# Kernel tuning notes

Measured on AMD Instinct MI355X. Metric: run time of the kernel, lower is better.

## Reference

```python
import jax, jax.numpy as jnp
import numpy as np

NEG = 0.01  # LeakyReLU default slope
EPS = 1e-5  # InstanceNorm eps

def conv(x, w, b=None, pad=0, groups=1):
    y = jax.lax.conv_general_dilated(x, w, (1, 1), [(pad, pad), (pad, pad)],
                                     dimension_numbers=('NCHW', 'OIHW', 'NCHW'),
                                     feature_group_count=groups)
    if b is not None:
        y = y + b[None, :, None, None]
    return y

def inorm(x):
    m = jnp.mean(x, axis=(2, 3), keepdims=True)
    v = jnp.var(x, axis=(2, 3), keepdims=True)
    return (x - m) / jnp.sqrt(v + EPS)

def lrelu(x):
    return jax.nn.leaky_relu(x, NEG)

def maxpool2(x):
    return jax.lax.reduce_window(x, -jnp.inf, jax.lax.max, (1, 1, 2, 2), (1, 1, 2, 2), 'VALID')

def setup_inputs() -> dict:
    key = jax.random.key(0)
    ks = jax.random.split(key, 17)
    C = 64
    def w(k, shape, fan_in):
        return (jax.random.normal(k, shape, jnp.float32) * (1.0 / np.sqrt(fan_in)))
    return {
        'x': jax.random.normal(ks[0], (4, 3, 256, 256), jnp.float32),
        'w_proj': w(ks[1], (C, 3, 3, 3), 27), 'b_proj': jnp.zeros((C,), jnp.float32),
        'w_a1': w(ks[2], (C // 4, C, 1, 1), C), 'w_a2': w(ks[3], (C, C // 4, 1, 1), C // 4),
        'w_ref': w(ks[4], (C, 1, 3, 3), 9), 'b_ref': jnp.zeros((C,), jnp.float32),
        'w_fuse': w(ks[5], (C, C, 1, 1), C), 'b_fuse': jnp.zeros((C,), jnp.float32),
        'w_con': w(ks[6], (2 * C * 4, 1, 3, 3), 9),
        'w_u1': w(ks[7], (C, 2 * C * 4, 1, 1), 2 * C * 4), 'b_u1': jnp.zeros((C,), jnp.float32),
        'w_u2': w(ks[8], (C, C, 3, 3), 9 * C), 'b_u2': jnp.zeros((C,), jnp.float32),
        'w_sc': w(ks[9], (C, 2 * C, 1, 1), 2 * C), 'b_sc': jnp.zeros((C,), jnp.float32),
    }

def reference(x, w_proj, b_proj, w_a1, w_a2, w_ref, b_ref, w_fuse, b_fuse,
              w_con, w_u1, b_u1, w_u2, b_u2, w_sc, b_sc):
    xp = conv(x, w_proj, b_proj, pad=1)
    B, C, H, W = xp.shape
    # --- high branch: pywt wavedec2+waverec2 is perfect reconstruction (identity);
    #     torch code detaches -> stop_gradient on the reconstruction path
    xw = jax.lax.stop_gradient(xp)
    a = jnp.mean(xw, axis=(2, 3), keepdims=True)          # AdaptiveAvgPool2d(1)
    a = lrelu(conv(a, w_a1))
    a = jax.nn.sigmoid(conv(a, w_a2))
    xw = xw * a
    xw = conv(xw, w_ref, b_ref, pad=1, groups=C)          # depthwise refine
    xw = lrelu(inorm(xw))
    # --- low branch: FFT low-pass box filter
    f = jnp.fft.fftshift(jnp.fft.fft2(xp), axes=(-2, -1))
    hl = int(H * 0.3 // 2); wl = int(W * 0.3 // 2)
    hc, wc = H // 2, W // 2
    mask = jnp.zeros((H, W), bool).at[hc - hl:hc + hl, wc - wl:wc + wl].set(True)
    low = jnp.fft.ifft2(jnp.fft.ifftshift(f * mask, axes=(-2, -1))).real
    low = lrelu(inorm(conv(low, w_fuse, b_fuse)))
    # --- hypergraph construct / unwrap
    xc = jnp.concatenate([xw, low], axis=1)               # [B, 2C, H, W]
    h = conv(xc, w_con, pad=1, groups=2 * C)              # [B, 2C*k, H, W]
    u = lrelu(inorm(conv(h, w_u1, b_u1)))
    u = lrelu(inorm(conv(u, w_u2, b_u2, pad=1)))
    feat = u + conv(xc, w_sc, b_sc)
    pooled = maxpool2(feat)
    return feat, pooled
```

## Files before the change

kernel.cpp:

```cpp
#include <hip/hip_runtime.h>
#include <hip/hip_bf16.h>

#define WIDTH 256
#define HW 65536
#define IMG 16777216
#define NIMG 256
#define NSPLIT 16

typedef __attribute__((ext_vector_type(8))) short bf8v;
typedef __attribute__((ext_vector_type(4))) float f4v;

__device__ __forceinline__ float lrelu_f(float v){ return v > 0.f ? v : 0.01f*v; }
__device__ __forceinline__ unsigned short bf16u(float v){
    __hip_bfloat16 h = __float2bfloat16(v);
    return *(unsigned short*)&h;
}

__global__ __launch_bounds__(256) void k_statsf(const float* __restrict__ ps, float* __restrict__ st)
{
    const int img = threadIdx.x;
    const float* p = ps + blockIdx.x * (256 * NSPLIT * 2) + img * (NSPLIT * 2);
    float* o = st + blockIdx.x * 512;
    float S = 0.f, S2 = 0.f;
#pragma unroll
    for (int q = 0; q < NSPLIT; q++) { S += p[q * 2]; S2 += p[q * 2 + 1]; }
    const float m = S / 65536.f;
    const float var = S2 / 65536.f - m * m;
    o[img * 2]     = m;
    o[img * 2 + 1] = rsqrtf(var + 1e-5f);
}

__global__ __launch_bounds__(256) void k_attention(const float* __restrict__ ps0,
    const float* __restrict__ wa1, const float* __restrict__ wa2, float* __restrict__ a2o)
{
    __shared__ float means[256];
    __shared__ float a1s[64];
    const int tid = threadIdx.x;
    {
        const float* p = ps0 + tid * (NSPLIT * 2);
        float S = 0.f;
#pragma unroll
        for (int q = 0; q < NSPLIT; q++) S += p[q * 2];
        means[tid] = S * (1.f / 65536.f);
    }
    __syncthreads();
    if (tid < 64) {
        const int b = tid >> 4, o = tid & 15;
        float s = 0.f;
        for (int c = 0; c < 64; c++) s += wa1[o * 64 + c] * means[b * 64 + c];
        a1s[b * 16 + o] = lrelu_f(s);
    }
    __syncthreads();
    {
        const int b = tid >> 6, c = tid & 63;
        float s = 0.f;
#pragma unroll
        for (int o = 0; o < 16; o++) s += wa2[c * 16 + o] * a1s[b * 16 + o];
        a2o[tid] = 1.f / (1.f + expf(-s));
    }
}

__global__ __launch_bounds__(256, 3) void k_proj(const float* __restrict__ x,
    const float* __restrict__ wt, const float* __restrict__ bias,
    float* __restrict__ out, float* __restrict__ ps0)
{
    __shared__ float wl[3][9][32];
    const int tid = threadIdx.x;
    const int og = tid >> 5, xg = tid & 31;
    const int half = blockIdx.x & 1;
    const int y = (blockIdx.x >> 1) & 255;
    const int b = blockIdx.x >> 9;
    const int o_base = half * 32;
    const int o0l = og * 4;
    const int x0 = xg * 8;
    const int split = y & (NSPLIT - 1);

    for (int idx = tid; idx < 3 * 9 * 32; idx += 256) {
        const int o = idx & 31;
        const int rest = idx >> 5;
        const int pos = rest % 9, cc = rest / 9;
        wl[cc][pos][o] = wt[((o_base + o) * 3 + cc) * 9 + pos];
    }
    __syncthreads();

    float acc[4][8];
#pragma unroll
    for (int i = 0; i < 4; i++)
#pragma unroll
        for (int j = 0; j < 8; j++) acc[i][j] = 0.f;

#pragma unroll 2
    for (int cc = 0; cc < 3; cc++) {
        const float* src = x + ((size_t)b * 3 + cc) * HW;
#pragma unroll
        for (int dy = 0; dy < 3; dy++) {
            const int yy = y + dy - 1;
            float vv[10];
            if (yy >= 0 && yy < 256) {
                const float* r = src + (size_t)yy * WIDTH;
                vv[0] = (x0 > 0) ? r[x0 - 1] : 0.f;
                const float4 m0 = *(const float4*)(r + x0);
                const float4 m1 = *(const float4*)(r + x0 + 4);
                vv[1] = m0.x; vv[2] = m0.y; vv[3] = m0.z; vv[4] = m0.w;
                vv[5] = m1.x; vv[6] = m1.y; vv[7] = m1.z; vv[8] = m1.w;
                vv[9] = (x0 < 248) ? r[x0 + 8] : 0.f;
            } else {
#pragma unroll
                for (int q = 0; q < 10; q++) vv[q] = 0.f;
            }
#pragma unroll
            for (int dx = 0; dx < 3; dx++) {
                const float4 w4 = *(const float4*)&wl[cc][dy * 3 + dx][o0l];
                const float wv[4] = { w4.x, w4.y, w4.z, w4.w };
#pragma unroll
                for (int oi = 0; oi < 4; oi++)
#pragma unroll
                    for (int px = 0; px < 8; px++)
                        acc[oi][px] += wv[oi] * vv[px + dx];
            }
        }
    }
#pragma unroll
    for (int oi = 0; oi < 4; oi++) {
        const int o = o_base + o0l + oi;
        const float bv = bias[o];
        const size_t off = ((size_t)(b * 64 + o)) * HW + (size_t)y * WIDTH + x0;
        float4 r0, r1;
        r0.x = acc[oi][0] + bv; r0.y = acc[oi][1] + bv; r0.z = acc[oi][2] + bv; r0.w = acc[oi][3] + bv;
        r1.x = acc[oi][4] + bv; r1.y = acc[oi][5] + bv; r1.z = acc[oi][6] + bv; r1.w = acc[oi][7] + bv;
        *(float4*)(out + off) = r0;
        *(float4*)(out + off + 4) = r1;
        float s  = r0.x + r0.y + r0.z + r0.w + r1.x + r1.y + r1.z + r1.w;
        float s2 = r0.x*r0.x + r0.y*r0.y + r0.z*r0.z + r0.w*r0.w
                 + r1.x*r1.x + r1.y*r1.y + r1.z*r1.z + r1.w*r1.w;
#pragma unroll
        for (int offt = 16; offt > 0; offt >>= 1) {
            s  += __shfl_down(s, offt, 32);
            s2 += __shfl_down(s2, offt, 32);
        }
        if (xg == 0) {
            float* pp = &ps0[((b * 64 + o) * NSPLIT + split) * 2];
            atomicAdd(pp, s);
            atomicAdd(pp + 1, s2);
        }
    }
}

__global__ __launch_bounds__(256) void k_dw(const float* __restrict__ xp, const float* __restrict__ a2,
    const float* __restrict__ wref, const float* __restrict__ bref, float* __restrict__ out,
    float* __restrict__ ps1)
{
    const int tid = threadIdx.x;
    const int img = blockIdx.x >> 6;
    const int y = ((blockIdx.x & 63) << 2) + (tid >> 6);
    const int x0 = (tid & 63) * 4;
    const int c = img & 63;
    const int split = blockIdx.x & (NSPLIT - 1);
    const float* src = xp + (size_t)img * HW;
    float wv[9];
#pragma unroll
    for (int k = 0; k < 9; k++) wv[k] = wref[c * 9 + k];
    const float scale = a2[img], bb = bref[c];

    float a[4] = {0.f, 0.f, 0.f, 0.f};
#pragma unroll
    for (int dy = 0; dy < 3; dy++) {
        const int yy = y + dy - 1;
        if (yy < 0 || yy > 255) continue;
        const float* r = src + (size_t)yy * WIDTH;
        float vv[6];
        vv[0] = (x0 > 0) ? r[x0 - 1] : 0.f;
        const float4 m = *(const float4*)(r + x0);
        vv[1] = m.x; vv[2] = m.y; vv[3] = m.z; vv[4] = m.w;
        vv[5] = (x0 < 252) ? r[x0 + 4] : 0.f;
#pragma unroll
        for (int dx = 0; dx < 3; dx++)
#pragma unroll
            for (int px = 0; px < 4; px++)
                a[px] += wv[dy * 3 + dx] * vv[px + dx];
    }
    float4 o;
    o.x = bb + scale * a[0]; o.y = bb + scale * a[1];
    o.z = bb + scale * a[2]; o.w = bb + scale * a[3];
    *(float4*)(out + (size_t)img * HW + (size_t)y * WIDTH + x0) = o;

    float s  = o.x + o.y + o.z + o.w;
    float s2 = o.x*o.x + o.y*o.y + o.z*o.z + o.w*o.w;
#pragma unroll
    for (int offt = 32; offt > 0; offt >>= 1) {
        s  += __shfl_down(s, offt, 64);
        s2 += __shfl_down(s2, offt, 64);
    }
    __shared__ float ls[4][2];
    const int wid = tid >> 6, lane = tid & 63;
    if (lane == 0) { ls[wid][0] = s; ls[wid][1] = s2; }
    __syncthreads();
    if (tid == 0) {
        const float S  = ls[0][0] + ls[1][0] + ls[2][0] + ls[3][0];
        const float S2 = ls[0][1] + ls[1][1] + ls[2][1] + ls[3][1];
        float* pp = &ps1[(img * NSPLIT + split) * 2];
        atomicAdd(pp, S);
        atomicAdd(pp + 1, S2);
    }
}

__global__ void k_tables(float* __restrict__ kr2, float* __restrict__ ki2)
{
    const int t = blockIdx.x * 256 + threadIdx.x;
    if (t < 512) {
        const int tm = t & 255;
        const double PI = 3.14159265358979323846;
        const double th = 2.0 * PI * (double)tm / 256.0;
        double sr = 1.0;
        for (int k = 1; k <= 37; k++) sr += 2.0 * cos((double)k * th);
        sr += cos(38.0 * th);
        kr2[t] = (float)(sr / 256.0);
        ki2[t] = (float)(-sin(38.0 * th) / 256.0);
    }
}

__global__ __launch_bounds__(256) void k_kmat(const float* __restrict__ kr2, const float* __restrict__ ki2,
    unsigned short* __restrict__ KBr, unsigned short* __restrict__ KBi)
{
    const int n = blockIdx.x, k = threadIdx.x;
    const int d = (n - k) & 255;
    KBr[n * 256 + k] = bf16u(kr2[d]);
    KBi[n * 256 + k] = bf16u(ki2[d]);
}

__global__ __launch_bounds__(256, 2) void k_mdft1(const float* __restrict__ xp,
    const unsigned short* __restrict__ KBr, const unsigned short* __restrict__ KBi,
    unsigned short* __restrict__ TR, unsigned short* __restrict__ TI)
{
    const int tid = threadIdx.x, lane = tid & 63, wave = tid >> 6;
    const int img = blockIdx.x >> 2;
    const int mb = (blockIdx.x >> 1) & 1, nb = blockIdx.x & 1;
    const int M0 = mb * 128 + (wave >> 1) * 64;
    const int N0 = nb * 128 + (wave & 1) * 64;
    const int lrow = lane & 15, lk = lane >> 4;
    const float* Xb = xp + (size_t)img * HW;

    f4v aR[4][4], aI[4][4];
#pragma unroll
    for (int m = 0; m < 4; m++)
#pragma unroll
        for (int n = 0; n < 4; n++) { aR[m][n] = (f4v){0,0,0,0}; aI[m][n] = (f4v){0,0,0,0}; }

#pragma unroll 1
    for (int k0 = 0; k0 < 256; k0 += 32) {
        bf8v af[4];
#pragma unroll
        for (int m = 0; m < 4; m++) {
            const float* rp = Xb + (size_t)(M0 + m * 16 + lrow) * 256 + k0 + lk * 8;
            const float4 a0 = *(const float4*)rp;
            const float4 a1 = *(const float4*)(rp + 4);
            bf8v t;
            t[0] = (short)bf16u(a0.x); t[1] = (short)bf16u(a0.y);
            t[2] = (short)bf16u(a0.z); t[3] = (short)bf16u(a0.w);
            t[4] = (short)bf16u(a1.x); t[5] = (short)bf16u(a1.y);
            t[6] = (short)bf16u(a1.z); t[7] = (short)bf16u(a1.w);
            af[m] = t;
        }
#pragma unroll
        for (int n = 0; n < 4; n++) {
            const int xcol = N0 + n * 16 + lrow;
            const bf8v br = *(const bf8v*)(KBr + xcol * 256 + k0 + lk * 8);
            const bf8v bi = *(const bf8v*)(KBi + xcol * 256 + k0 + lk * 8);
#pragma unroll
            for (int m = 0; m < 4; m++) {
                aR[m][n] = __builtin_amdgcn_mfma_f32_16x16x32_bf16(af[m], br, aR[m][n], 0, 0, 0);
                aI[m][n] = __builtin_amdgcn_mfma_f32_16x16x32_bf16(af[m], bi, aI[m][n], 0, 0, 0);
            }
        }
    }
#pragma unroll
    for (int n = 0; n < 4; n++) {
        const size_t xoff = (size_t)img * HW + (size_t)(N0 + n * 16 + lrow) * 256;
#pragma unroll
        for (int m = 0; m < 4; m++) {
            const size_t off = xoff + M0 + m * 16 + lk * 4;
            const f4v r = aR[m][n], ii = aI[m][n];
            ushort4 ur, ui;
            ur.x = bf16u(r[0]); ur.y = bf16u(r[1]); ur.z = bf16u(r[2]); ur.w = bf16u(r[3]);
            ui.x = bf16u(ii[0]); ui.y = bf16u(ii[1]); ui.z = bf16u(ii[2]); ui.w = bf16u(ii[3]);
            *(ushort4*)(TR + off) = ur;
            *(ushort4*)(TI + off) = ui;
        }
    }
}

__global__ __launch_bounds__(256, 2) void k_mdft2(const unsigned short* __restrict__ TR,
    const unsigned short* __restrict__ TI, const unsigned short* __restrict__ KBr,
    const unsigned short* __restrict__ KBi, float* __restrict__ low)
{
    const int tid = threadIdx.x, lane = tid & 63, wave = tid >> 6;
    const int img = blockIdx.x >> 2;
    const int mb = (blockIdx.x >> 1) & 1, nb = blockIdx.x & 1;
    const int M0 = mb * 128 + (wave >> 1) * 64;
    const int N0 = nb * 128 + (wave & 1) * 64;
    const int lrow = lane & 15, lk = lane >> 4;
    const unsigned short* TRb = TR + (size_t)img * HW;
    const unsigned short* TIb = TI + (size_t)img * HW;

    f4v aR[4][4], aI[4][4];
#pragma unroll
    for (int m = 0; m < 4; m++)
#pragma unroll
        for (int n = 0; n < 4; n++) { aR[m][n] = (f4v){0,0,0,0}; aI[m][n] = (f4v){0,0,0,0}; }

#pragma unroll 1
    for (int k0 = 0; k0 < 256; k0 += 32) {
        bf8v afR[4], afI[4];
#pragma unroll
        for (int m = 0; m < 4; m++) {
            const int ro = (M0 + m * 16 + lrow) * 256 + k0 + lk * 8;
            afR[m] = *(const bf8v*)(TRb + ro);
            afI[m] = *(const bf8v*)(TIb + ro);
        }
#pragma unroll
        for (int n = 0; n < 4; n++) {
            const int ycol = N0 + n * 16 + lrow;
            const bf8v br = *(const bf8v*)(KBr + ycol * 256 + k0 + lk * 8);
            const bf8v bi = *(const bf8v*)(KBi + ycol * 256 + k0 + lk * 8);
#pragma unroll
            for (int m = 0; m < 4; m++) {
                aR[m][n] = __builtin_amdgcn_mfma_f32_16x16x32_bf16(afR[m], br, aR[m][n], 0, 0, 0);
                aI[m][n] = __builtin_amdgcn_mfma_f32_16x16x32_bf16(afI[m], bi, aI[m][n], 0, 0, 0);
            }
        }
    }
#pragma unroll
    for (int n = 0; n < 4; n++) {
        const size_t yoff = (size_t)img * HW + (size_t)(N0 + n * 16 + lrow) * 256;
#pragma unroll
        for (int m = 0; m < 4; m++) {
            const f4v r = aR[m][n], ii = aI[m][n];
            const float4 v = make_float4(r[0] - ii[0], r[1] - ii[1], r[2] - ii[2], r[3] - ii[3]);
            *(float4*)(low + yoff + M0 + m * 16 + lk * 4) = v;
        }
    }
}

__global__ __launch_bounds__(256) void k_weff_bf(const float* __restrict__ w_u1,
    const float* __restrict__ w_con, unsigned short* __restrict__ wbf)
{
    const int f = blockIdx.x * 256 + threadIdx.x;
    if (f >= 73728) return;
    const int ch = f & 31, oc = (f >> 5) & 63, cp = f >> 11;
    const int pos = cp % 9, cb = cp / 9;
    const int g = cb * 32 + ch;
    float s = 0.f;
#pragma unroll
    for (int j = 0; j < 4; j++) s += w_u1[oc * 512 + g * 4 + j] * w_con[(g * 4 + j) * 9 + pos];
    wbf[f] = bf16u(s);
}

template<int CIN>
__global__ __launch_bounds__(256) void k_wcvt(const float* __restrict__ w, unsigned short* __restrict__ wbf)
{
    const int f = blockIdx.x * 256 + threadIdx.x;
    if (f >= 64 * CIN * 9) return;
    const int ch = f & 31, oc = (f >> 5) & 63, cp = f >> 11;
    const int pos = cp % 9, cb = cp / 9;
    const int c = cb * 32 + ch;
    wbf[f] = bf16u(w[oc * CIN * 9 + c * 9 + pos]);
}

template<int CIN>
__global__ __launch_bounds__(256) void k_wcvt1(const float* __restrict__ w, unsigned short* __restrict__ wbf)
{
    const int f = blockIdx.x * 256 + threadIdx.x;
    if (f >= 64 * CIN) return;
    const int ch = f & 31, oc = (f >> 5) & 63, cb = f >> 11;
    wbf[f] = bf16u(w[oc * CIN + cb * 32 + ch]);
}

template<int CIN>
__global__ __launch_bounds__(256, 2) void k_mconv(
    const float* __restrict__ in0, const float* __restrict__ in1,
    const unsigned short* __restrict__ wbf, const float* __restrict__ bias,
    float* __restrict__ out,
    const float* __restrict__ stA, const float* __restrict__ stB,
    float* __restrict__ psOut)
{
    __shared__ unsigned short Xl[4 * 260 * 32];
    __shared__ float sh_ms[64];
    __shared__ float red[4][64][2];
    const int tid = threadIdx.x;
    const int lane = tid & 63;
    const int wave = tid >> 6;
    const int b = blockIdx.x >> 7;
    const int y0 = (blockIdx.x & 127) * 2;
    const int row_sel = wave >> 1;
    const int px_base = (wave & 1) * 128;
    const int split = blockIdx.x & (NSPLIT - 1);

    for (int i = tid; i < 4 * 260 * 32 / 2; i += 256) ((unsigned int*)Xl)[i] = 0u;

    f4v acc[8][4];
#pragma unroll
    for (int i = 0; i < 8; i++)
#pragma unroll
        for (int n = 0; n < 4; n++) acc[i][n] = (f4v){0.f, 0.f, 0.f, 0.f};

    const int pxl   = px_base + (lane & 15);
    const int gsl   = lane >> 4;
    const int wlane = (lane & 15) * 32 + gsl * 8;

    constexpr int NC = CIN / 32;
#pragma unroll 1
    for (int cb = 0; cb < NC; cb++) {
        const int c0 = cb * 32;
        const bool second = (CIN == 128 && c0 >= 64);
        const float* src = (second ? in1 : in0) + ((size_t)b * 64 + (c0 & 63)) * HW;
        const float* st = second ? stB : stA;
        __syncthreads();
        if (tid < 32) {
            const int img = b * 64 + (c0 & 63) + tid;
            sh_ms[tid * 2]     = st[img * 2];
            sh_ms[tid * 2 + 1] = st[img * 2 + 1];
        }
        __syncthreads();
        {
            const int px = tid;
            const int px_idx = px + 1;
            const int sw = (px_idx >> 1) & 3;
#pragma unroll 1
            for (int r = 0; r < 4; r++) {
                const int yy = y0 - 1 + r;
                if (yy < 0 || yy > 255) continue;
                const float* rp = src + (size_t)yy * WIDTH + px;
#pragma unroll 4
                for (int d = 0; d < 16; d++) {
                    float va = rp[(size_t)(2 * d) * HW];
                    float vb = rp[(size_t)(2 * d + 1) * HW];
                    va = lrelu_f((va - sh_ms[4 * d])     * sh_ms[4 * d + 1]);
                    vb = lrelu_f((vb - sh_ms[4 * d + 2]) * sh_ms[4 * d + 3]);
                    const unsigned int dw = (unsigned int)bf16u(va)
                                          | ((unsigned int)bf16u(vb) << 16);
                    const int byte = r * 16640 + px_idx * 64
                                   + (((d >> 2) ^ sw) << 4) + ((d & 3) << 2);
                    *(unsigned int*)((char*)Xl + byte) = dw;
                }
            }
        }
        __syncthreads();
#pragma unroll 1
        for (int pos = 0; pos < 9; pos++) {
            const int dy = pos / 3, dx = pos - dy * 3;
            const unsigned short* wp = wbf + (cb * 9 + pos) * 2048 + wlane;
            const bf8v wf0 = *(const bf8v*)(wp);
            const bf8v wf1 = *(const bf8v*)(wp + 512);
            const bf8v wf2 = *(const bf8v*)(wp + 1024);
            const bf8v wf3 = *(const bf8v*)(wp + 1536);
            const int pxe = pxl + dx;
            const int row = row_sel + dy;
            const char* abase = (const char*)Xl + row * 16640 + pxe * 64
                              + ((gsl ^ ((pxe >> 1) & 3)) << 4);
#pragma unroll
            for (int i = 0; i < 8; i++) {
                const bf8v af = *(const bf8v*)(abase + i * 1024);
                acc[i][0] = __builtin_amdgcn_mfma_f32_16x16x32_bf16(af, wf0, acc[i][0], 0, 0, 0);
                acc[i][1] = __builtin_amdgcn_mfma_f32_16x16x32_bf16(af, wf1, acc[i][1], 0, 0, 0);
                acc[i][2] = __builtin_amdgcn_mfma_f32_16x16x32_bf16(af, wf2, acc[i][2], 0, 0, 0);
                acc[i][3] = __builtin_amdgcn_mfma_f32_16x16x32_bf16(af, wf3, acc[i][3], 0, 0, 0);
            }
        }
    }
    const int yrow = y0 + row_sel;
    const int lrow = lane & 15, lk = lane >> 4;
#pragma unroll
    for (int n = 0; n < 4; n++) {
        const float bv = bias[n * 16 + lrow];
        float* po = out + ((size_t)(b * 64) + n * 16 + lrow) * HW
                  + (size_t)yrow * WIDTH + px_base + lk * 4;
        float s = 0.f, s2 = 0.f;
#pragma unroll
        for (int i = 0; i < 8; i++) {
            const f4v a = acc[i][n];
            float4 v;
            v.x = a[0] + bv; v.y = a[1] + bv; v.z = a[2] + bv; v.w = a[3] + bv;
            s  += v.x + v.y + v.z + v.w;
            s2 += v.x*v.x + v.y*v.y + v.z*v.z + v.w*v.w;
            *(float4*)(po + i * 16) = v;
        }
        s  += __shfl_down(s, 32);  s  += __shfl_down(s, 16);
        s2 += __shfl_down(s2, 32); s2 += __shfl_down(s2, 16);
        if (lk == 0) { red[wave][n * 16 + lrow][0] = s; red[wave][n * 16 + lrow][1] = s2; }
    }
    __syncthreads();
    if (tid < 64) {
        const float S  = red[0][tid][0] + red[1][tid][0] + red[2][tid][0] + red[3][tid][0];
        const float S2 = red[0][tid][1] + red[1][tid][1] + red[2][tid][1] + red[3][tid][1];
        float* pp = &psOut[((b * 64 + tid) * NSPLIT + split) * 2];
        atomicAdd(pp, S);
        atomicAdd(pp + 1, S2);
    }
}

template<int CIN, bool ADD, bool NORMIN, bool STATS>
__global__ __launch_bounds__(256, 2) void k_pconv(
    const float* __restrict__ in0, const float* __restrict__ in1,
    const unsigned short* __restrict__ wbf, const float* __restrict__ bias,
    const float* __restrict__ addsrc, float* __restrict__ out,
    const float* __restrict__ stA, const float* __restrict__ stB,
    const float* __restrict__ stAdd, float* __restrict__ psOut)
{
    __shared__ unsigned short Xl[256 * 32];
    __shared__ float sh_ms[64];
    __shared__ float red[4][64][2];
    const int tid = threadIdx.x, lane = tid & 63, wave = tid >> 6;
    const int y = blockIdx.x & 255, b = blockIdx.x >> 8;
    const int split = blockIdx.x & (NSPLIT - 1);
    const int lrow = lane & 15, gsl = lane >> 4;
    const int wpx = wave * 64;
    const int wlane = lrow * 32 + gsl * 8;

    f4v acc[4][4];
#pragma unroll
    for (int m = 0; m < 4; m++)
#pragma unroll
        for (int n = 0; n < 4; n++) acc[m][n] = (f4v){0.f, 0.f, 0.f, 0.f};

    constexpr int NC = CIN / 32;
#pragma unroll 1
    for (int cb = 0; cb < NC; cb++) {
        const int c0 = cb * 32;
        const bool second = (CIN == 128 && c0 >= 64);
        const float* src = (second ? in1 : in0) + ((size_t)b * 64 + (c0 & 63)) * HW
                         + (size_t)y * WIDTH;
        __syncthreads();
        if (NORMIN && tid < 32) {
            const float* st = second ? stB : stA;
            const int img = b * 64 + (c0 & 63) + tid;
            sh_ms[tid * 2]     = st[img * 2];
            sh_ms[tid * 2 + 1] = st[img * 2 + 1];
        }
        __syncthreads();
        {
            const int px = tid;
            const int sw = (px >> 1) & 3;
#pragma unroll 4
            for (int d = 0; d < 16; d++) {
                float va = src[(size_t)(2 * d) * HW + px];
                float vb = src[(size_t)(2 * d + 1) * HW + px];
                if constexpr (NORMIN) {
                    va = lrelu_f((va - sh_ms[4 * d])     * sh_ms[4 * d + 1]);
                    vb = lrelu_f((vb - sh_ms[4 * d + 2]) * sh_ms[4 * d + 3]);
                }
                const unsigned int dw = (unsigned int)bf16u(va)
                                      | ((unsigned int)bf16u(vb) << 16);
                const int byte = px * 64 + (((d >> 2) ^ sw) << 4) + ((d & 3) << 2);
                *(unsigned int*)((char*)Xl + byte) = dw;
            }
        }
        __syncthreads();
        {
            const unsigned short* wp = wbf + cb * 2048 + wlane;
            const bf8v wf0 = *(const bf8v*)(wp);
            const bf8v wf1 = *(const bf8v*)(wp + 512);
            const bf8v wf2 = *(const bf8v*)(wp + 1024);
            const bf8v wf3 = *(const bf8v*)(wp + 1536);
#pragma unroll
            for (int m = 0; m < 4; m++) {
                const int px = wpx + m * 16 + lrow;
                const char* abase = (const char*)Xl + px * 64
                                  + ((gsl ^ ((px >> 1) & 3)) << 4);
                const bf8v af = *(const bf8v*)abase;
                acc[m][0] = __builtin_amdgcn_mfma_f32_16x16x32_bf16(af, wf0, acc[m][0], 0, 0, 0);
                acc[m][1] = __builtin_amdgcn_mfma_f32_16x16x32_bf16(af, wf1, acc[m][1], 0, 0, 0);
                acc[m][2] = __builtin_amdgcn_mfma_f32_16x16x32_bf16(af, wf2, acc[m][2], 0, 0, 0);
                acc[m][3] = __builtin_amdgcn_mfma_f32_16x16x32_bf16(af, wf3, acc[m][3], 0, 0, 0);
            }
        }
    }
    const int lk = gsl;
#pragma unroll
    for (int n = 0; n < 4; n++) {
        const int oc = n * 16 + lrow;
        const float bv = bias[oc];
        float mm = 0.f, ss = 0.f;
        if constexpr (ADD) { mm = stAdd[(b * 64 + oc) * 2]; ss = stAdd[(b * 64 + oc) * 2 + 1]; }
        const size_t orow = ((size_t)(b * 64 + oc)) * HW + (size_t)y * WIDTH;
        float s = 0.f, s2 = 0.f;
#pragma unroll
        for (int m = 0; m < 4; m++) {
            const int px = wpx + m * 16 + lk * 4;
            const f4v a = acc[m][n];
            float r[4] = { a[0] + bv, a[1] + bv, a[2] + bv, a[3] + bv };
            if constexpr (ADD) {
                const float4 av = *(const float4*)(addsrc + orow + px);
                r[0] += lrelu_f((av.x - mm) * ss);
                r[1] += lrelu_f((av.y - mm) * ss);
                r[2] += lrelu_f((av.z - mm) * ss);
                r[3] += lrelu_f((av.w - mm) * ss);
            }
            *(float4*)(out + orow + px) = make_float4(r[0], r[1], r[2], r[3]);
            if constexpr (STATS) {
                s  += r[0] + r[1] + r[2] + r[3];
                s2 += r[0]*r[0] + r[1]*r[1] + r[2]*r[2] + r[3]*r[3];
            }
        }
        if constexpr (STATS) {
            s  += __shfl_down(s, 32);  s  += __shfl_down(s, 16);
            s2 += __shfl_down(s2, 32); s2 += __shfl_down(s2, 16);
            if (lk == 0) { red[wave][oc][0] = s; red[wave][oc][1] = s2; }
        }
    }
    if constexpr (STATS) {
        __syncthreads();
        if (tid < 64) {
            const float S  = red[0][tid][0] + red[1][tid][0] + red[2][tid][0] + red[3][tid][0];
            const float S2 = red[0][tid][1] + red[1][tid][1] + red[2][tid][1] + red[3][tid][1];
            float* pp = &psOut[((b * 64 + tid) * NSPLIT + split) * 2];
            atomicAdd(pp, S);
            atomicAdd(pp + 1, S2);
        }
    }
}

__global__ __launch_bounds__(256) void k_maxpool(const float* __restrict__ feat, float* __restrict__ out)
{
    const int idx = blockIdx.x * 256 + threadIdx.x;
    const int xo = idx & 127;
    const int yo = (idx >> 7) & 127;
    const int img = idx >> 14;
    const float* p = feat + (size_t)img * HW + (size_t)(yo * 2) * WIDTH + xo * 2;
    out[idx] = fmaxf(fmaxf(p[0], p[1]), fmaxf(p[WIDTH], p[WIDTH + 1]));
}

extern "C" void kernel_launch(void* const* d_in, const int* in_sizes, int n_in,
                              void* d_out, int out_size, void* d_ws, size_t ws_size,
                              hipStream_t stream)
{
    const float* x      = (const float*)d_in[0];
    const float* w_proj = (const float*)d_in[1];
    const float* b_proj = (const float*)d_in[2];
    const float* w_a1   = (const float*)d_in[3];
    const float* w_a2   = (const float*)d_in[4];
    const float* w_ref  = (const float*)d_in[5];
    const float* b_ref  = (const float*)d_in[6];
    const float* w_fuse = (const float*)d_in[7];
    const float* b_fuse = (const float*)d_in[8];
    const float* w_con  = (const float*)d_in[9];
    const float* w_u1   = (const float*)d_in[10];
    const float* b_u1   = (const float*)d_in[11];
    const float* w_u2   = (const float*)d_in[12];
    const float* b_u2   = (const float*)d_in[13];
    const float* w_sc   = (const float*)d_in[14];
    const float* b_sc   = (const float*)d_in[15];

    float* wsf  = (float*)d_ws;
    float* buf0 = wsf;
    float* buf1 = wsf + (size_t)IMG;
    float* buf2 = wsf + (size_t)2 * IMG;
    float* aux  = wsf + (size_t)3 * IMG;
    float* a2b  = aux;
    float* kr2  = aux + 256;
    float* ki2  = aux + 768;
    unsigned short* wbfA = (unsigned short*)(aux + 1280);
    unsigned short* wbfB = wbfA + 73728;
    unsigned short* KBr  = wbfB + 36864;
    unsigned short* KBi  = KBr + 65536;
    unsigned short* wbfF = KBi + 65536;
    unsigned short* wbfS = wbfF + 4096;
    float* ps   = aux + 1280 + 120832 + 6144;
    float* st   = ps + 5 * 256 * NSPLIT * 2;

    float* fout = (float*)d_out;
    float* pout = fout + (size_t)IMG;
    unsigned short* T1R = (unsigned short*)buf2;
    unsigned short* T1I = T1R + (size_t)IMG;

    const int PSSLOT = 256 * NSPLIT * 2;

    hipMemsetAsync(ps, 0, 5 * PSSLOT * sizeof(float), stream);
    k_tables<<<2, 256, 0, stream>>>(kr2, ki2);
    k_kmat<<<256, 256, 0, stream>>>(kr2, ki2, KBr, KBi);
    k_weff_bf<<<288, 256, 0, stream>>>(w_u1, w_con, wbfA);
    k_wcvt<64><<<144, 256, 0, stream>>>(w_u2, wbfB);
    k_wcvt1<64><<<16, 256, 0, stream>>>(w_fuse, wbfF);
    k_wcvt1<128><<<32, 256, 0, stream>>>(w_sc, wbfS);
    k_proj<<<2048, 256, 0, stream>>>(x, w_proj, b_proj, buf0, ps);
    k_attention<<<1, 256, 0, stream>>>(ps, w_a1, w_a2, a2b);
    k_dw<<<16384, 256, 0, stream>>>(buf0, a2b, w_ref, b_ref, buf1, ps + PSSLOT);
    k_mdft1<<<1024, 256, 0, stream>>>(buf0, KBr, KBi, T1R, T1I);
    k_mdft2<<<1024, 256, 0, stream>>>(T1R, T1I, KBr, KBi, fout);
    k_pconv<64, false, false, true><<<1024, 256, 0, stream>>>(
        fout, nullptr, wbfF, b_fuse, nullptr, buf0,
        nullptr, nullptr, nullptr, ps + 2 * PSSLOT);
    k_statsf<<<2, 256, 0, stream>>>(ps + PSSLOT, st + 512);
    k_mconv<128><<<512, 256, 0, stream>>>(buf1, buf0, wbfA, b_u1, fout,
        st + 512, st + 1024, ps + 3 * PSSLOT);
    k_statsf<<<1, 256, 0, stream>>>(ps + 3 * PSSLOT, st + 1536);
    k_mconv<64><<<512, 256, 0, stream>>>(fout, nullptr, wbfB, b_u2, buf2,
        st + 1536, st + 1536, ps + 4 * PSSLOT);
    k_statsf<<<1, 256, 0, stream>>>(ps + 4 * PSSLOT, st + 2048);
    k_pconv<128, true, true, false><<<1024, 256, 0, stream>>>(
        buf1, buf0, wbfS, b_sc, buf2, fout,
        st + 512, st + 1024, st + 2048, nullptr);
    k_maxpool<<<16384, 256, 0, stream>>>(fout, pout);
}
```

Baseline: 493.3 us.

## Halve mconv tile width, raise occupancy, preload norm stats once

k_mconv now processes half a row (128 px) per block with a 130-pixel halo tile, halving accumulators and LDS so launch bounds can allow 4 blocks per CU, and the grid doubles to 1024 blocks. Both mconv and pconv load all per-channel mean/scale stats into shared memory once up front, which removes two barriers per channel block and leaves one barrier at the end of each iteration. Narrower tiles re-read halo columns, and only two of four thread groups' row slots are used per staging pass, which may lower load efficiency.

```diff
diff --git a/kernel.cpp b/kernel.cpp
--- a/kernel.cpp
+++ b/kernel.cpp
@@ -376,36 +376,45 @@
 }
 
 template<int CIN>
-__global__ __launch_bounds__(256, 2) void k_mconv(
+__global__ __launch_bounds__(256, 4) void k_mconv(
     const float* __restrict__ in0, const float* __restrict__ in1,
     const unsigned short* __restrict__ wbf, const float* __restrict__ bias,
     float* __restrict__ out,
     const float* __restrict__ stA, const float* __restrict__ stB,
     float* __restrict__ psOut)
 {
-    __shared__ unsigned short Xl[4 * 260 * 32];
-    __shared__ float sh_ms[64];
+    __shared__ unsigned short Xl[4 * 132 * 32];
+    __shared__ float sh_ms[2 * CIN];
     __shared__ float red[4][64][2];
     const int tid = threadIdx.x;
     const int lane = tid & 63;
     const int wave = tid >> 6;
-    const int b = blockIdx.x >> 7;
-    const int y0 = (blockIdx.x & 127) * 2;
+    const int xb = (blockIdx.x & 1) * 128;
+    const int y0 = ((blockIdx.x >> 1) & 127) * 2;
+    const int b = blockIdx.x >> 8;
     const int row_sel = wave >> 1;
-    const int px_base = (wave & 1) * 128;
+    const int px_half = (wave & 1) * 64;
     const int split = blockIdx.x & (NSPLIT - 1);
 
-    for (int i = tid; i < 4 * 260 * 32 / 2; i += 256) ((unsigned int*)Xl)[i] = 0u;
-
-    f4v acc[8][4];
-#pragma unroll
-    for (int i = 0; i < 8; i++)
+    for (int i = tid; i < 4 * 132 * 32 / 2; i += 256) ((unsigned int*)Xl)[i] = 0u;
+    for (int j = tid; j < 2 * CIN; j += 256) {
+        const int cb_ = j >> 6, jj = j & 63;
+        const int c = cb_ * 32 + 2 * (jj >> 2) + ((jj & 3) >> 1);
+        const float* st = (CIN == 128 && cb_ >= 2) ? stB : stA;
+        sh_ms[j] = st[(b * 64 + (c & 63)) * 2 + (jj & 1)];
+    }
+
+    f4v acc[4][4];
+#pragma unroll
+    for (int i = 0; i < 4; i++)
 #pragma unroll
         for (int n = 0; n < 4; n++) acc[i][n] = (f4v){0.f, 0.f, 0.f, 0.f};
 
-    const int pxl   = px_base + (lane & 15);
-    const int gsl   = lane >> 4;
-    const int wlane = (lane & 15) * 32 + gsl * 8;
+    const int lrow = lane & 15;
+    const int gsl  = lane >> 4;
+    const int wlane = lrow * 32 + gsl * 8;
+
+    __syncthreads();
 
     constexpr int NC = CIN / 32;
 #pragma unroll 1
@@ -413,34 +422,30 @@
         const int c0 = cb * 32;
         const bool second = (CIN == 128 && c0 >= 64);
         const float* src = (second ? in1 : in0) + ((size_t)b * 64 + (c0 & 63)) * HW;
-        const float* st = second ? stB : stA;
-        __syncthreads();
-        if (tid < 32) {
-            const int img = b * 64 + (c0 & 63) + tid;
-            sh_ms[tid * 2]     = st[img * 2];
-            sh_ms[tid * 2 + 1] = st[img * 2 + 1];
-        }
-        __syncthreads();
+        const float* ms = sh_ms + cb * 64;
         {
-            const int px = tid;
-            const int px_idx = px + 1;
-            const int sw = (px_idx >> 1) & 3;
+            const int r = tid >> 6;
+            const int yy = y0 - 1 + r;
+            if (yy >= 0 && yy <= 255) {
 #pragma unroll 1
-            for (int r = 0; r < 4; r++) {
-                const int yy = y0 - 1 + r;
-                if (yy < 0 || yy > 255) continue;
-                const float* rp = src + (size_t)yy * WIDTH + px;
+                for (int s = tid & 63; s < 130; s += 64) {
+                    const int x = xb + s - 1;
+                    if (x >= 0 && x <= 255) {
+                        const float* rp = src + (size_t)yy * WIDTH + x;
+                        const int sbase = r * 8448 + s * 64;
+                        const int sw = (s >> 1) & 3;
 #pragma unroll 4
-                for (int d = 0; d < 16; d++) {
-                    float va = rp[(size_t)(2 * d) * HW];
-                    float vb = rp[(size_t)(2 * d + 1) * HW];
-                    va = lrelu_f((va - sh_ms[4 * d])     * sh_ms[4 * d + 1]);
-                    vb = lrelu_f((vb - sh_ms[4 * d + 2]) * sh_ms[4 * d + 3]);
-                    const unsigned int dw = (unsigned int)bf16u(va)
-                                          | ((unsigned int)bf16u(vb) << 16);
-                    const int byte = r * 16640 + px_idx * 64
-                                   + (((d >> 2) ^ sw) << 4) + ((d & 3) << 2);
-                    *(unsigned int*)((char*)Xl + byte) = dw;
+                        for (int d = 0; d < 16; d++) {
+                            float va = rp[(size_t)(2 * d) * HW];
+                            float vb = rp[(size_t)(2 * d + 1) * HW];
+                            va = lrelu_f((va - ms[4 * d])     * ms[4 * d + 1]);
+                            vb = lrelu_f((vb - ms[4 * d + 2]) * ms[4 * d + 3]);
+                            const unsigned int dw = (unsigned int)bf16u(va)
+                                                  | ((unsigned int)bf16u(vb) << 16);
+                            *(unsigned int*)((char*)Xl + sbase
+                                + (((d >> 2) ^ sw) << 4) + ((d & 3) << 2)) = dw;
+                        }
+                    }
                 }
             }
         }
@@ -453,12 +458,12 @@
             const bf8v wf1 = *(const bf8v*)(wp + 512);
             const bf8v wf2 = *(const bf8v*)(wp + 1024);
             const bf8v wf3 = *(const bf8v*)(wp + 1536);
-            const int pxe = pxl + dx;
+            const int pxe = px_half + lrow + dx;
             const int row = row_sel + dy;
-            const char* abase = (const char*)Xl + row * 16640 + pxe * 64
+            const char* abase = (const char*)Xl + row * 8448 + pxe * 64
                               + ((gsl ^ ((pxe >> 1) & 3)) << 4);
 #pragma unroll
-            for (int i = 0; i < 8; i++) {
+            for (int i = 0; i < 4; i++) {
                 const bf8v af = *(const bf8v*)(abase + i * 1024);
                 acc[i][0] = __builtin_amdgcn_mfma_f32_16x16x32_bf16(af, wf0, acc[i][0], 0, 0, 0);
                 acc[i][1] = __builtin_amdgcn_mfma_f32_16x16x32_bf16(af, wf1, acc[i][1], 0, 0, 0);
@@ -466,17 +471,18 @@
                 acc[i][3] = __builtin_amdgcn_mfma_f32_16x16x32_bf16(af, wf3, acc[i][3], 0, 0, 0);
             }
         }
+        __syncthreads();
     }
     const int yrow = y0 + row_sel;
-    const int lrow = lane & 15, lk = lane >> 4;
+    const int lk = gsl;
 #pragma unroll
     for (int n = 0; n < 4; n++) {
         const float bv = bias[n * 16 + lrow];
         float* po = out + ((size_t)(b * 64) + n * 16 + lrow) * HW
-                  + (size_t)yrow * WIDTH + px_base + lk * 4;
+                  + (size_t)yrow * WIDTH + xb + px_half + lk * 4;
         float s = 0.f, s2 = 0.f;
 #pragma unroll
-        for (int i = 0; i < 8; i++) {
+        for (int i = 0; i < 4; i++) {
             const f4v a = acc[i][n];
             float4 v;
             v.x = a[0] + bv; v.y = a[1] + bv; v.z = a[2] + bv; v.w = a[3] + bv;
@@ -499,7 +505,7 @@
 }
 
 template<int CIN, bool ADD, bool NORMIN, bool STATS>
-__global__ __launch_bounds__(256, 2) void k_pconv(
+__global__ __launch_bounds__(256, 3) void k_pconv(
     const float* __restrict__ in0, const float* __restrict__ in1,
     const unsigned short* __restrict__ wbf, const float* __restrict__ bias,
     const float* __restrict__ addsrc, float* __restrict__ out,
@@ -507,7 +513,7 @@
     const float* __restrict__ stAdd, float* __restrict__ psOut)
 {
     __shared__ unsigned short Xl[256 * 32];
-    __shared__ float sh_ms[64];
+    __shared__ float sh_ms[2 * CIN];
     __shared__ float red[4][64][2];
     const int tid = threadIdx.x, lane = tid & 63, wave = tid >> 6;
     const int y = blockIdx.x & 255, b = blockIdx.x >> 8;
@@ -516,11 +522,22 @@
     const int wpx = wave * 64;
     const int wlane = lrow * 32 + gsl * 8;
 
+    if constexpr (NORMIN) {
+        for (int j = tid; j < 2 * CIN; j += 256) {
+            const int cb_ = j >> 6, jj = j & 63;
+            const int c = cb_ * 32 + 2 * (jj >> 2) + ((jj & 3) >> 1);
+            const float* st = (CIN == 128 && cb_ >= 2) ? stB : stA;
+            sh_ms[j] = st[(b * 64 + (c & 63)) * 2 + (jj & 1)];
+        }
+    }
+
     f4v acc[4][4];
 #pragma unroll
     for (int m = 0; m < 4; m++)
 #pragma unroll
         for (int n = 0; n < 4; n++) acc[m][n] = (f4v){0.f, 0.f, 0.f, 0.f};
+
+    __syncthreads();
 
     constexpr int NC = CIN / 32;
 #pragma unroll 1
@@ -529,14 +546,7 @@
         const bool second = (CIN == 128 && c0 >= 64);
         const float* src = (second ? in1 : in0) + ((size_t)b * 64 + (c0 & 63)) * HW
                          + (size_t)y * WIDTH;
-        __syncthreads();
-        if (NORMIN && tid < 32) {
-            const float* st = second ? stB : stA;
-            const int img = b * 64 + (c0 & 63) + tid;
-            sh_ms[tid * 2]     = st[img * 2];
-            sh_ms[tid * 2 + 1] = st[img * 2 + 1];
-        }
-        __syncthreads();
+        const float* ms = sh_ms + cb * 64;
         {
             const int px = tid;
             const int sw = (px >> 1) & 3;
@@ -545,8 +555,8 @@
                 float va = src[(size_t)(2 * d) * HW + px];
                 float vb = src[(size_t)(2 * d + 1) * HW + px];
                 if constexpr (NORMIN) {
-                    va = lrelu_f((va - sh_ms[4 * d])     * sh_ms[4 * d + 1]);
-                    vb = lrelu_f((vb - sh_ms[4 * d + 2]) * sh_ms[4 * d + 3]);
+                    va = lrelu_f((va - ms[4 * d])     * ms[4 * d + 1]);
+                    vb = lrelu_f((vb - ms[4 * d + 2]) * ms[4 * d + 3]);
                 }
                 const unsigned int dw = (unsigned int)bf16u(va)
                                       | ((unsigned int)bf16u(vb) << 16);
@@ -573,6 +583,7 @@
                 acc[m][3] = __builtin_amdgcn_mfma_f32_16x16x32_bf16(af, wf3, acc[m][3], 0, 0, 0);
             }
         }
+        __syncthreads();
     }
     const int lk = gsl;
 #pragma unroll
@@ -690,10 +701,10 @@
         fout, nullptr, wbfF, b_fuse, nullptr, buf0,
         nullptr, nullptr, nullptr, ps + 2 * PSSLOT);
     k_statsf<<<2, 256, 0, stream>>>(ps + PSSLOT, st + 512);
-    k_mconv<128><<<512, 256, 0, stream>>>(buf1, buf0, wbfA, b_u1, fout,
+    k_mconv<128><<<1024, 256, 0, stream>>>(buf1, buf0, wbfA, b_u1, fout,
         st + 512, st + 1024, ps + 3 * PSSLOT);
     k_statsf<<<1, 256, 0, stream>>>(ps + 3 * PSSLOT, st + 1536);
-    k_mconv<64><<<512, 256, 0, stream>>>(fout, nullptr, wbfB, b_u2, buf2,
+    k_mconv<64><<<1024, 256, 0, stream>>>(fout, nullptr, wbfB, b_u2, buf2,
         st + 1536, st + 1536, ps + 4 * PSSLOT);
     k_statsf<<<1, 256, 0, stream>>>(ps + 4 * PSSLOT, st + 2048);
     k_pconv<128, true, true, false><<<1024, 256, 0, stream>>>(
```

After: 543.6 us. 1.1x slower.
